# Optimization experiments

Hardware: AMD Instinct MI355X
Metric: run time of the kernel (lower is better)

Reference implementation:

```python
import jax, jax.numpy as jnp
import numpy as np

V, H, O = 32, 256, 256  # input_dim, hidden_dim, output_dim
EPS = 1e-5


def _layer_norm(x, g, b):
    m = jnp.mean(x, axis=-1, keepdims=True)
    v = jnp.mean((x - m) ** 2, axis=-1, keepdims=True)
    return g * (x - m) * jax.lax.rsqrt(v + EPS) + b


def setup_inputs() -> dict:
    key = jax.random.key(0)
    ks = jax.random.split(key, 20)
    s = 0.05
    inp = {
        "x": jax.random.normal(ks[0], (16, 256, V), dtype=jnp.float32),
        # selection GRN (input_dim -> input_dim, identity skip)
        "sel_fc1_w": jax.random.normal(ks[1], (V, H), dtype=jnp.float32) * s,
        "sel_fc1_b": jnp.zeros((H,), jnp.float32),
        "sel_fc2_w": jax.random.normal(ks[2], (H, V), dtype=jnp.float32) * s,
        "sel_fc2_b": jnp.zeros((V,), jnp.float32),
        "sel_gate_w": jax.random.normal(ks[3], (V, 2 * V), dtype=jnp.float32) * s,
        "sel_gate_b": jnp.zeros((2 * V,), jnp.float32),
        "sel_ln_g": jnp.ones((V,), jnp.float32),
        "sel_ln_b": jnp.zeros((V,), jnp.float32),
        # per-variable GRNs, stacked over the V variables (each has in_dim=1)
        "var_fc1_w": jax.random.normal(ks[4], (V, H), dtype=jnp.float32) * s,
        "var_fc1_b": jnp.zeros((V, H), jnp.float32),
        "var_fc2_w": jax.random.normal(ks[5], (V, H, O), dtype=jnp.float32) * s,
        "var_fc2_b": jnp.zeros((V, O), jnp.float32),
        "var_gate_w": jax.random.normal(ks[6], (V, 2 * O), dtype=jnp.float32) * s,
        "var_gate_b": jnp.zeros((V, 2 * O), jnp.float32),
        "var_skip_w": jax.random.normal(ks[7], (V, O), dtype=jnp.float32) * s,
        "var_skip_b": jnp.zeros((V, O), jnp.float32),
        "var_ln_g": jnp.ones((V, O), jnp.float32),
        "var_ln_b": jnp.zeros((V, O), jnp.float32),
    }
    return inp


def _vsn_forward(x, sel_fc1_w, sel_fc1_b, sel_fc2_w, sel_fc2_b, sel_gate_w,
                 sel_gate_b, sel_ln_g, sel_ln_b, var_fc1_w, var_fc1_b,
                 var_fc2_w, var_fc2_b, var_gate_w, var_gate_b, var_skip_w,
                 var_skip_b, var_ln_g, var_ln_b):
    B, S, _ = x.shape
    xr = x.reshape(-1, V)  # [N, V]

    # --- selection GRN (skip is identity) ---
    h = jax.nn.elu(xr @ sel_fc1_w + sel_fc1_b)        # [N, H]
    h = h @ sel_fc2_w + sel_fc2_b                      # [N, V] (unused by residual; matches torch code)
    g = xr @ sel_gate_w + sel_gate_b                   # [N, 2V]
    gates, values = jnp.split(g, 2, axis=-1)
    glu = jax.nn.sigmoid(gates) * values               # [N, V]
    sel = _layer_norm(glu + xr, sel_ln_g, sel_ln_b)    # [N, V]
    weights = jax.nn.softmax(sel, axis=-1)             # [N, V]

    # --- batched per-variable GRNs (in_dim = 1) ---
    xv = xr[..., None]                                  # [N, V, 1]
    hv = jax.nn.elu(xv * var_fc1_w + var_fc1_b)         # [N, V, H]
    hv = jnp.einsum('nvh,vho->nvo', hv, var_fc2_w) + var_fc2_b  # [N, V, O]
    gv = xv * var_gate_w + var_gate_b                   # [N, V, 2O]
    gates_v, values_v = jnp.split(gv, 2, axis=-1)
    glu_v = jax.nn.sigmoid(gates_v) * values_v          # [N, V, O]
    skip_v = xv * var_skip_w + var_skip_b               # [N, V, O]
    proc = _layer_norm(glu_v + skip_v, var_ln_g, var_ln_b)  # [N, V, O]

    out = jnp.einsum('nv,nvo->no', weights, proc)       # [N, O]
    return out.reshape(B, S, O)


def reference(x, sel_fc1_w, sel_fc1_b, sel_fc2_w, sel_fc2_b, sel_gate_w,
              sel_gate_b, sel_ln_g, sel_ln_b, var_fc1_w, var_fc1_b,
              var_fc2_w, var_fc2_b, var_gate_w, var_gate_b, var_skip_w,
              var_skip_b, var_ln_g, var_ln_b):
    return _vsn_forward(x, sel_fc1_w, sel_fc1_b, sel_fc2_w, sel_fc2_b,
                        sel_gate_w, sel_gate_b, sel_ln_g, sel_ln_b,
                        var_fc1_w, var_fc1_b, var_fc2_w, var_fc2_b,
                        var_gate_w, var_gate_b, var_skip_w, var_skip_b,
                        var_ln_g, var_ln_b)
```

## Files before the change

kernel.cpp:

```cpp
#include <hip/hip_runtime.h>
#include <hip/hip_bf16.h>


#define VDIM 32
#define ODIM 256
#define RPB  4
#define TPB  256

__device__ __forceinline__ float fast_sigmoid(float g) {
    return __builtin_amdgcn_rcpf(1.0f + __expf(-g));
}

__global__ void __launch_bounds__(TPB, 4) vsn_fused(
    const float* __restrict__ x,
    const float* __restrict__ sgw,
    const float* __restrict__ sgb,
    const float* __restrict__ slg,
    const float* __restrict__ slb,
    const float* __restrict__ vgw,
    const float* __restrict__ vgb,
    const float* __restrict__ vsw,
    const float* __restrict__ vsb,
    const float* __restrict__ vlg,
    const float* __restrict__ vlb,
    float* __restrict__ out)
{
    __shared__ float x_s[RPB][VDIM];
    __shared__ float g_s[RPB][2 * VDIM];
    __shared__ float w_s[RPB][VDIM];

    const int tid  = threadIdx.x;
    const int row0 = blockIdx.x * RPB;

    if (tid < RPB * VDIM)
        ((float*)x_s)[tid] = x[row0 * VDIM + tid];
    __syncthreads();

    {
        const int r = tid >> 6, j = tid & 63;
        float acc = sgb[j];
        #pragma unroll
        for (int v = 0; v < VDIM; ++v)
            acc = fmaf(x_s[r][v], sgw[v * 64 + j], acc);
        g_s[r][j] = acc;
    }
    __syncthreads();

    if (tid < RPB * VDIM) {
        const int r = tid >> 5, v = tid & 31;
        const float gate = g_s[r][v];
        const float val  = g_s[r][VDIM + v];
        const float y    = fast_sigmoid(gate) * val + x_s[r][v];
        float s1 = y, s2 = y * y;
        #pragma unroll
        for (int m = 1; m < 32; m <<= 1) {
            s1 += __shfl_xor(s1, m, 64);
            s2 += __shfl_xor(s2, m, 64);
        }
        const float mean = s1 * (1.0f / VDIM);
        const float var  = s2 * (1.0f / VDIM) - mean * mean;
        const float rs   = __builtin_amdgcn_rsqf(var + 1e-5f);
        const float sel  = slg[v] * ((y - mean) * rs) + slb[v];
        float mx = sel;
        #pragma unroll
        for (int m = 1; m < 32; m <<= 1)
            mx = fmaxf(mx, __shfl_xor(mx, m, 64));
        const float e = __expf(sel - mx);
        float se = e;
        #pragma unroll
        for (int m = 1; m < 32; m <<= 1)
            se += __shfl_xor(se, m, 64);
        w_s[r][v] = e * __builtin_amdgcn_rcpf(se);
    }
    __syncthreads();

    const int wave = tid >> 6;
    const int lane = tid & 63;
    const int o0   = lane << 2;
    const int row  = wave;

    float acc0 = 0.0f, acc1 = 0.0f, acc2 = 0.0f, acc3 = 0.0f;

    #pragma unroll 2
    for (int v = 0; v < VDIM; ++v) {
        const float4 ga  = *(const float4*)(vgw + v * 512 + o0);
        const float4 va  = *(const float4*)(vgw + v * 512 + 256 + o0);
        const float4 gab = *(const float4*)(vgb + v * 512 + o0);
        const float4 vab = *(const float4*)(vgb + v * 512 + 256 + o0);
        const float4 sw4 = *(const float4*)(vsw + v * 256 + o0);
        const float4 sb4 = *(const float4*)(vsb + v * 256 + o0);
        const float4 lg4 = *(const float4*)(vlg + v * 256 + o0);
        const float4 lb4 = *(const float4*)(vlb + v * 256 + o0);

        const float xv = x_s[row][v];

        const float y0 = fast_sigmoid(fmaf(xv, ga.x, gab.x)) * fmaf(xv, va.x, vab.x) + fmaf(xv, sw4.x, sb4.x);
        const float y1 = fast_sigmoid(fmaf(xv, ga.y, gab.y)) * fmaf(xv, va.y, vab.y) + fmaf(xv, sw4.y, sb4.y);
        const float y2 = fast_sigmoid(fmaf(xv, ga.z, gab.z)) * fmaf(xv, va.z, vab.z) + fmaf(xv, sw4.z, sb4.z);
        const float y3 = fast_sigmoid(fmaf(xv, ga.w, gab.w)) * fmaf(xv, va.w, vab.w) + fmaf(xv, sw4.w, sb4.w);

        float s1 = (y0 + y1) + (y2 + y3);
        float s2 = fmaf(y0, y0, fmaf(y1, y1, fmaf(y2, y2, y3 * y3)));
        #pragma unroll
        for (int m = 1; m < 64; m <<= 1) {
            s1 += __shfl_xor(s1, m, 64);
            s2 += __shfl_xor(s2, m, 64);
        }
        const float mean = s1 * (1.0f / ODIM);
        const float var  = s2 * (1.0f / ODIM) - mean * mean;
        const float rs   = __builtin_amdgcn_rsqf(var + 1e-5f);
        const float wv   = w_s[row][v];
        const float wrs  = wv * rs;
        acc0 = fmaf(lg4.x, (y0 - mean) * wrs, fmaf(wv, lb4.x, acc0));
        acc1 = fmaf(lg4.y, (y1 - mean) * wrs, fmaf(wv, lb4.y, acc1));
        acc2 = fmaf(lg4.z, (y2 - mean) * wrs, fmaf(wv, lb4.z, acc2));
        acc3 = fmaf(lg4.w, (y3 - mean) * wrs, fmaf(wv, lb4.w, acc3));
    }

    float4 o4 = make_float4(acc0, acc1, acc2, acc3);
    *(float4*)(out + (size_t)(row0 + row) * ODIM + o0) = o4;
}

extern "C" void kernel_launch(void* const* d_in, const int* in_sizes, int n_in,
                              void* d_out, int out_size, void* d_ws, size_t ws_size,
                              hipStream_t stream) {
    const float* x   = (const float*)d_in[0];
    const float* sgw = (const float*)d_in[5];
    const float* sgb = (const float*)d_in[6];
    const float* slg = (const float*)d_in[7];
    const float* slb = (const float*)d_in[8];
    const float* vgw = (const float*)d_in[13];
    const float* vgb = (const float*)d_in[14];
    const float* vsw = (const float*)d_in[15];
    const float* vsb = (const float*)d_in[16];
    const float* vlg = (const float*)d_in[17];
    const float* vlb = (const float*)d_in[18];
    float* out = (float*)d_out;

    const int N = in_sizes[0] / VDIM;
    const int grid = N / RPB;

    vsn_fused<<<grid, TPB, 0, stream>>>(x, sgw, sgb, slg, slb,
                                        vgw, vgb, vsw, vsb, vlg, vlb, out);
}
```

Before: 127.9 us.

## Stage per-variable weights in double-buffered LDS shared across 16 rows

Grows the block to 1024 threads handling 16 rows. All threads cooperatively load the per-variable gate, skip and layer-norm parameters into a double-buffered shared-memory tile, two variables at a time. Each wave then reads its parameters from LDS instead of global memory. The next chunk is prefetched into registers while the current chunk is computed, which cuts repeated global/L2 parameter reads by sharing them across 16 rows. In exchange it adds a block-wide barrier per chunk and leaves fewer, larger blocks per CU.

```diff
diff --git a/kernel.cpp b/kernel.cpp
--- a/kernel.cpp
+++ b/kernel.cpp
@@ -4,14 +4,16 @@
 
 #define VDIM 32
 #define ODIM 256
-#define RPB  4
-#define TPB  256
+#define RPB  16
+#define TPB  1024
+#define CHUNK_V 2
+#define NCHUNK  16
 
 __device__ __forceinline__ float fast_sigmoid(float g) {
     return __builtin_amdgcn_rcpf(1.0f + __expf(-g));
 }
 
-__global__ void __launch_bounds__(TPB, 4) vsn_fused(
+__global__ void __launch_bounds__(TPB) vsn_fused(
     const float* __restrict__ x,
     const float* __restrict__ sgw,
     const float* __restrict__ sgb,
@@ -25,12 +27,24 @@
     const float* __restrict__ vlb,
     float* __restrict__ out)
 {
+    __shared__ float wbuf[2][4096];
     __shared__ float x_s[RPB][VDIM];
     __shared__ float g_s[RPB][2 * VDIM];
     __shared__ float w_s[RPB][VDIM];
 
     const int tid  = threadIdx.x;
     const int row0 = blockIdx.x * RPB;
+
+    const float* sbase;
+    int sstr;
+    if (tid < 256)      { sbase = vgw + (tid << 2);         sstr = 1024; }
+    else if (tid < 512) { sbase = vgb + ((tid - 256) << 2); sstr = 1024; }
+    else if (tid < 640) { sbase = vsw + ((tid - 512) << 2); sstr = 512;  }
+    else if (tid < 768) { sbase = vsb + ((tid - 640) << 2); sstr = 512;  }
+    else if (tid < 896) { sbase = vlg + ((tid - 768) << 2); sstr = 512;  }
+    else                { sbase = vlb + ((tid - 896) << 2); sstr = 512;  }
+
+    const float4 st0 = *(const float4*)sbase;
 
     if (tid < RPB * VDIM)
         ((float*)x_s)[tid] = x[row0 * VDIM + tid];
@@ -45,6 +59,8 @@
         g_s[r][j] = acc;
     }
     __syncthreads();
+
+    ((float4*)wbuf[0])[tid & 1023] = st0;
 
     if (tid < RPB * VDIM) {
         const int r = tid >> 5, v = tid & 31;
@@ -77,48 +93,60 @@
     const int wave = tid >> 6;
     const int lane = tid & 63;
     const int o0   = lane << 2;
-    const int row  = wave;
 
     float acc0 = 0.0f, acc1 = 0.0f, acc2 = 0.0f, acc3 = 0.0f;
 
-    #pragma unroll 2
-    for (int v = 0; v < VDIM; ++v) {
-        const float4 ga  = *(const float4*)(vgw + v * 512 + o0);
-        const float4 va  = *(const float4*)(vgw + v * 512 + 256 + o0);
-        const float4 gab = *(const float4*)(vgb + v * 512 + o0);
-        const float4 vab = *(const float4*)(vgb + v * 512 + 256 + o0);
-        const float4 sw4 = *(const float4*)(vsw + v * 256 + o0);
-        const float4 sb4 = *(const float4*)(vsb + v * 256 + o0);
-        const float4 lg4 = *(const float4*)(vlg + v * 256 + o0);
-        const float4 lb4 = *(const float4*)(vlb + v * 256 + o0);
+    for (int c = 0; c < NCHUNK; ++c) {
+        float4 pf;
+        if (c < NCHUNK - 1)
+            pf = *(const float4*)(sbase + (c + 1) * sstr);
 
-        const float xv = x_s[row][v];
+        const float* buf = wbuf[c & 1];
 
-        const float y0 = fast_sigmoid(fmaf(xv, ga.x, gab.x)) * fmaf(xv, va.x, vab.x) + fmaf(xv, sw4.x, sb4.x);
-        const float y1 = fast_sigmoid(fmaf(xv, ga.y, gab.y)) * fmaf(xv, va.y, vab.y) + fmaf(xv, sw4.y, sb4.y);
-        const float y2 = fast_sigmoid(fmaf(xv, ga.z, gab.z)) * fmaf(xv, va.z, vab.z) + fmaf(xv, sw4.z, sb4.z);
-        const float y3 = fast_sigmoid(fmaf(xv, ga.w, gab.w)) * fmaf(xv, va.w, vab.w) + fmaf(xv, sw4.w, sb4.w);
+        #pragma unroll
+        for (int v4 = 0; v4 < CHUNK_V; ++v4) {
+            const int v = c * CHUNK_V + v4;
+            const float4 ga  = *(const float4*)(buf + v4 * 512 + o0);
+            const float4 va  = *(const float4*)(buf + v4 * 512 + 256 + o0);
+            const float4 gab = *(const float4*)(buf + 1024 + v4 * 512 + o0);
+            const float4 vab = *(const float4*)(buf + 1024 + v4 * 512 + 256 + o0);
+            const float4 sw4 = *(const float4*)(buf + 2048 + v4 * 256 + o0);
+            const float4 sb4 = *(const float4*)(buf + 2560 + v4 * 256 + o0);
+            const float4 lg4 = *(const float4*)(buf + 3072 + v4 * 256 + o0);
+            const float4 lb4 = *(const float4*)(buf + 3584 + v4 * 256 + o0);
 
-        float s1 = (y0 + y1) + (y2 + y3);
-        float s2 = fmaf(y0, y0, fmaf(y1, y1, fmaf(y2, y2, y3 * y3)));
-        #pragma unroll
-        for (int m = 1; m < 64; m <<= 1) {
-            s1 += __shfl_xor(s1, m, 64);
-            s2 += __shfl_xor(s2, m, 64);
+            const float xv = x_s[wave][v];
+
+            const float y0 = fast_sigmoid(fmaf(xv, ga.x, gab.x)) * fmaf(xv, va.x, vab.x) + fmaf(xv, sw4.x, sb4.x);
+            const float y1 = fast_sigmoid(fmaf(xv, ga.y, gab.y)) * fmaf(xv, va.y, vab.y) + fmaf(xv, sw4.y, sb4.y);
+            const float y2 = fast_sigmoid(fmaf(xv, ga.z, gab.z)) * fmaf(xv, va.z, vab.z) + fmaf(xv, sw4.z, sb4.z);
+            const float y3 = fast_sigmoid(fmaf(xv, ga.w, gab.w)) * fmaf(xv, va.w, vab.w) + fmaf(xv, sw4.w, sb4.w);
+
+            float s1 = (y0 + y1) + (y2 + y3);
+            float s2 = fmaf(y0, y0, fmaf(y1, y1, fmaf(y2, y2, y3 * y3)));
+            #pragma unroll
+            for (int m = 1; m < 64; m <<= 1) {
+                s1 += __shfl_xor(s1, m, 64);
+                s2 += __shfl_xor(s2, m, 64);
+            }
+            const float mean = s1 * (1.0f / ODIM);
+            const float var  = s2 * (1.0f / ODIM) - mean * mean;
+            const float rs   = __builtin_amdgcn_rsqf(var + 1e-5f);
+            const float wv   = w_s[wave][v];
+            const float wrs  = wv * rs;
+            acc0 = fmaf(lg4.x, (y0 - mean) * wrs, fmaf(wv, lb4.x, acc0));
+            acc1 = fmaf(lg4.y, (y1 - mean) * wrs, fmaf(wv, lb4.y, acc1));
+            acc2 = fmaf(lg4.z, (y2 - mean) * wrs, fmaf(wv, lb4.z, acc2));
+            acc3 = fmaf(lg4.w, (y3 - mean) * wrs, fmaf(wv, lb4.w, acc3));
         }
-        const float mean = s1 * (1.0f / ODIM);
-        const float var  = s2 * (1.0f / ODIM) - mean * mean;
-        const float rs   = __builtin_amdgcn_rsqf(var + 1e-5f);
-        const float wv   = w_s[row][v];
-        const float wrs  = wv * rs;
-        acc0 = fmaf(lg4.x, (y0 - mean) * wrs, fmaf(wv, lb4.x, acc0));
-        acc1 = fmaf(lg4.y, (y1 - mean) * wrs, fmaf(wv, lb4.y, acc1));
-        acc2 = fmaf(lg4.z, (y2 - mean) * wrs, fmaf(wv, lb4.z, acc2));
-        acc3 = fmaf(lg4.w, (y3 - mean) * wrs, fmaf(wv, lb4.w, acc3));
+
+        if (c < NCHUNK - 1)
+            ((float4*)wbuf[(c + 1) & 1])[tid & 1023] = pf;
+        __syncthreads();
     }
 
     float4 o4 = make_float4(acc0, acc1, acc2, acc3);
-    *(float4*)(out + (size_t)(row0 + row) * ODIM + o0) = o4;
+    *(float4*)(out + (size_t)(row0 + wave) * ODIM + o0) = o4;
 }
 
 extern "C" void kernel_launch(void* const* d_in, const int* in_sizes, int n_in,
```

Result: faster. 125.2 us (-2.1%).
